# Optimization experiments

Measured on AMD Instinct MI355X. Metric: run time of the kernel, lower is better.

## Reference

```python
import jax, jax.numpy as jnp
import numpy as np

B, IN_SIZE, P = 16384, 4096, 8
D = IN_SIZE // P  # 512


def setup_inputs() -> dict:
    key = jax.random.key(0)
    ks = jax.random.split(key, 10)
    bound = 1.0 / np.sqrt(D)  # fan_in = int_dim
    return {
        "x": jax.random.normal(ks[0], (B, IN_SIZE), dtype=jnp.float32),
        "weights1": jax.random.uniform(ks[1], (P, D, D), jnp.float32, -bound, bound),
        "bias1": jax.random.uniform(ks[2], (IN_SIZE,), jnp.float32, -bound, bound),
        "weights2": jax.random.uniform(ks[3], (P, D, D), jnp.float32, -bound, bound),
        "bias2": jax.random.uniform(ks[4], (IN_SIZE,), jnp.float32, -bound, bound),
        # trainable swish params (init 0 as in torch code)
        "gamma1": jnp.zeros((IN_SIZE,), jnp.float32),
        "beta1": jnp.zeros((IN_SIZE,), jnp.float32),
        "gamma3": jnp.zeros((IN_SIZE,), jnp.float32),
        "beta3": jnp.zeros((IN_SIZE,), jnp.float32),
        # Affine norms (scalar gain/bias)
        "gain1": jnp.ones((1,), jnp.float32),
        "nbias1": jnp.zeros((1,), jnp.float32),
        "gain3": jnp.ones((1,), jnp.float32),
        "nbias3": jnp.zeros((1,), jnp.float32),
    }


def _swish(x, gamma, beta):
    # f(x) = (gamma + sigmoid(beta*x) * (1-gamma)) * x
    return (gamma + jax.nn.sigmoid(beta * x) * (1.0 - gamma)) * x


def _block_matmul(x, w):
    # x: [B, IN_SIZE] -> [B, P, D]; block-diagonal matmul == batched per-partition GEMM
    xb = x.reshape(x.shape[0], P, D)
    return jnp.einsum("bpd,pde->bpe", xb, w).reshape(x.shape[0], IN_SIZE)


def reference(x, weights1, bias1, weights2, bias2, gamma1, beta1, gamma3, beta3,
              gain1, nbias1, gain3, nbias3):
    o1 = _swish(_block_matmul(x * gain1 + nbias1, weights1) + bias1, gamma1, beta1)
    o2 = _swish(_block_matmul(o1 * gain3 + nbias3, weights2) + bias2, gamma3, beta3) + x
    return o2
```

## Files before the change

### kernel.cpp

```cpp
#include <hip/hip_runtime.h>
#include <cstdint>
#include <cstddef>


#define B_ROWS 16384
#define IN_SZ  4096
#define P_PART 8
#define D_DIM  512

typedef unsigned short ushort_t;
typedef __attribute__((ext_vector_type(8))) short short8;
typedef __attribute__((ext_vector_type(4))) float f32x4;

__device__ inline unsigned short f2bf(float f) {
  union { float f; unsigned int u; } c; c.f = f;
  unsigned int u = c.u;
  return (unsigned short)((u + 0x7fffu + ((u >> 16) & 1u)) >> 16);
}

__device__ inline void gld_to_lds16(const void* g, void* l) {
  __builtin_amdgcn_global_load_lds((const __attribute__((address_space(1))) void*)g,
                                   (__attribute__((address_space(3))) void*)l,
                                   16, 0, 0);
}

__global__ __launch_bounds__(256) void wconv_kernel(const float* __restrict__ w1,
                                                    const float* __restrict__ w2,
                                                    ushort_t* __restrict__ wt1,
                                                    ushort_t* __restrict__ wt2) {
  __shared__ float tile[64][68];
  const int p = blockIdx.z & 7;
  const float*  src = (blockIdx.z < 8) ? w1 : w2;
  ushort_t*     dst = (blockIdx.z < 8) ? wt1 : wt2;
  const int k0 = blockIdx.x * 64;
  const int n0 = blockIdx.y * 64;
  const int t = threadIdx.x;

  const float* base = src + ((size_t)p * D_DIM + k0) * D_DIM + n0;
#pragma unroll
  for (int i = 0; i < 4; ++i) {
    int f = t + i * 256;
    int kr = f >> 4;
    int c4 = f & 15;
    float4 v = *(const float4*)(base + (size_t)kr * D_DIM + c4 * 4);
    *(float4*)(&tile[kr][c4 * 4]) = v;
  }
  __syncthreads();
  ushort_t* obase = dst + ((size_t)p * D_DIM + n0) * D_DIM + k0;
#pragma unroll
  for (int i = 0; i < 4; ++i) {
    int f = t + i * 256;
    int nr = f >> 4;
    int kc = (f & 15) * 4;
    unsigned int lo = f2bf(tile[kc + 0][nr]) | ((unsigned int)f2bf(tile[kc + 1][nr]) << 16);
    unsigned int hi = f2bf(tile[kc + 2][nr]) | ((unsigned int)f2bf(tile[kc + 3][nr]) << 16);
    uint2 pk; pk.x = lo; pk.y = hi;
    *(uint2*)(obase + (size_t)nr * D_DIM + kc) = pk;
  }
}

__global__ __launch_bounds__(256) void gemm1_kernel(
    const float* __restrict__ x, const ushort_t* __restrict__ wt1,
    const float* __restrict__ bias1, const float* __restrict__ gamma1,
    const float* __restrict__ beta1,
    const float* __restrict__ gain1, const float* __restrict__ nbias1,
    const float* __restrict__ gain3, const float* __restrict__ nbias3,
    ushort_t* __restrict__ o1) {
  __shared__ __align__(16) ushort_t As[128 * 64];
  __shared__ __align__(16) ushort_t Bs[128 * 64];

  const int t = threadIdx.x;
  const int lane = t & 63, wid = t >> 6;
  const int wm = wid & 1, wn = wid >> 1;
  const int l15 = lane & 15, quad = lane >> 4;
  const int m0 = blockIdx.x * 128;
  const int n0 = blockIdx.y * 128;
  const int p  = blockIdx.z;

  const float g1 = gain1[0], nb1 = nbias1[0];
  const float g3 = gain3[0], nb3 = nbias3[0];

  f32x4 acc[4][4];
#pragma unroll
  for (int i = 0; i < 4; ++i)
#pragma unroll
    for (int j = 0; j < 4; ++j) acc[i][j] = (f32x4)(0.0f);

  const ushort_t* wbase = wt1 + (size_t)p * D_DIM * D_DIM;

  for (int kt = 0; kt < 8; ++kt) {
    __syncthreads();
    const float* xtile = x + (size_t)m0 * IN_SZ + p * D_DIM + kt * 64;
#pragma unroll
    for (int i = 0; i < 8; ++i) {
      int f = t + i * 256;
      int row = f >> 4, c4 = f & 15;
      float4 v = *(const float4*)(xtile + (size_t)row * IN_SZ + c4 * 4);
      v.x = v.x * g1 + nb1; v.y = v.y * g1 + nb1;
      v.z = v.z * g1 + nb1; v.w = v.w * g1 + nb1;
      uint2 pk;
      pk.x = f2bf(v.x) | ((unsigned int)f2bf(v.y) << 16);
      pk.y = f2bf(v.z) | ((unsigned int)f2bf(v.w) << 16);
      *(uint2*)(&As[f * 4]) = pk;
    }
#pragma unroll
    for (int c = 0; c < 4; ++c) {
      int off = (wid * 4 + c) * 1024;
      int lb = off + lane * 16;
      int n = lb >> 7, kb = lb & 127;
      const ushort_t* g = wbase + (size_t)(n0 + n) * D_DIM + kt * 64 + (kb >> 1);
      gld_to_lds16(g, (char*)Bs + off);
    }
    __syncthreads();
#pragma unroll
    for (int kk = 0; kk < 2; ++kk) {
      const int kof = kk * 32 + quad * 8;
      short8 a[4], b[4];
#pragma unroll
      for (int i = 0; i < 4; ++i)
        a[i] = *(const short8*)(&As[(wm * 64 + i * 16 + l15) * 64 + kof]);
#pragma unroll
      for (int j = 0; j < 4; ++j)
        b[j] = *(const short8*)(&Bs[(wn * 64 + j * 16 + l15) * 64 + kof]);
#pragma unroll
      for (int i = 0; i < 4; ++i)
#pragma unroll
        for (int j = 0; j < 4; ++j)
          acc[i][j] = __builtin_amdgcn_mfma_f32_16x16x32_bf16(a[i], b[j], acc[i][j], 0, 0, 0);
    }
  }

  const int colg0 = p * D_DIM + n0 + wn * 64;
  const int row0 = m0 + wm * 64 + quad * 4;
#pragma unroll
  for (int j = 0; j < 4; ++j) {
    int col = colg0 + j * 16 + l15;
    float bv = bias1[col], ga = gamma1[col], be = beta1[col];
#pragma unroll
    for (int i = 0; i < 4; ++i) {
      int r0 = row0 + i * 16;
#pragma unroll
      for (int r = 0; r < 4; ++r) {
        float v = acc[i][j][r] + bv;
        float sg = 1.0f / (1.0f + __expf(-be * v));
        float o = (ga + sg * (1.0f - ga)) * v;
        o = o * g3 + nb3;
        o1[(size_t)(r0 + r) * IN_SZ + col] = f2bf(o);
      }
    }
  }
}

__global__ __launch_bounds__(256) void gemm2_kernel(
    const ushort_t* __restrict__ o1, const ushort_t* __restrict__ wt2,
    const float* __restrict__ bias2, const float* __restrict__ gamma3,
    const float* __restrict__ beta3,
    const float* __restrict__ x, float* __restrict__ out) {
  __shared__ __align__(16) ushort_t As[128 * 64];
  __shared__ __align__(16) ushort_t Bs[128 * 64];

  const int t = threadIdx.x;
  const int lane = t & 63, wid = t >> 6;
  const int wm = wid & 1, wn = wid >> 1;
  const int l15 = lane & 15, quad = lane >> 4;
  const int m0 = blockIdx.x * 128;
  const int n0 = blockIdx.y * 128;
  const int p  = blockIdx.z;

  f32x4 acc[4][4];
#pragma unroll
  for (int i = 0; i < 4; ++i)
#pragma unroll
    for (int j = 0; j < 4; ++j) acc[i][j] = (f32x4)(0.0f);

  const ushort_t* wbase = wt2 + (size_t)p * D_DIM * D_DIM;

  for (int kt = 0; kt < 8; ++kt) {
    __syncthreads();
#pragma unroll
    for (int c = 0; c < 4; ++c) {
      int off = (wid * 4 + c) * 1024;
      int lb = off + lane * 16;
      int m = lb >> 7, kb = lb & 127;
      const ushort_t* g = o1 + (size_t)(m0 + m) * IN_SZ + p * D_DIM + kt * 64 + (kb >> 1);
      gld_to_lds16(g, (char*)As + off);
    }
#pragma unroll
    for (int c = 0; c < 4; ++c) {
      int off = (wid * 4 + c) * 1024;
      int lb = off + lane * 16;
      int n = lb >> 7, kb = lb & 127;
      const ushort_t* g = wbase + (size_t)(n0 + n) * D_DIM + kt * 64 + (kb >> 1);
      gld_to_lds16(g, (char*)Bs + off);
    }
    __syncthreads();
#pragma unroll
    for (int kk = 0; kk < 2; ++kk) {
      const int kof = kk * 32 + quad * 8;
      short8 a[4], b[4];
#pragma unroll
      for (int i = 0; i < 4; ++i)
        a[i] = *(const short8*)(&As[(wm * 64 + i * 16 + l15) * 64 + kof]);
#pragma unroll
      for (int j = 0; j < 4; ++j)
        b[j] = *(const short8*)(&Bs[(wn * 64 + j * 16 + l15) * 64 + kof]);
#pragma unroll
      for (int i = 0; i < 4; ++i)
#pragma unroll
        for (int j = 0; j < 4; ++j)
          acc[i][j] = __builtin_amdgcn_mfma_f32_16x16x32_bf16(a[i], b[j], acc[i][j], 0, 0, 0);
    }
  }

  const int colg0 = p * D_DIM + n0 + wn * 64;
  const int row0 = m0 + wm * 64 + quad * 4;
#pragma unroll
  for (int j = 0; j < 4; ++j) {
    int col = colg0 + j * 16 + l15;
    float bv = bias2[col], ga = gamma3[col], be = beta3[col];
#pragma unroll
    for (int i = 0; i < 4; ++i) {
      int r0 = row0 + i * 16;
#pragma unroll
      for (int r = 0; r < 4; ++r) {
        float v = acc[i][j][r] + bv;
        float sg = 1.0f / (1.0f + __expf(-be * v));
        float o = (ga + sg * (1.0f - ga)) * v;
        size_t idx = (size_t)(r0 + r) * IN_SZ + col;
        out[idx] = o + x[idx];
      }
    }
  }
}

extern "C" void kernel_launch(void* const* d_in, const int* in_sizes, int n_in,
                              void* d_out, int out_size, void* d_ws, size_t ws_size,
                              hipStream_t stream) {
  const float* x      = (const float*)d_in[0];
  const float* w1     = (const float*)d_in[1];
  const float* b1     = (const float*)d_in[2];
  const float* w2     = (const float*)d_in[3];
  const float* b2     = (const float*)d_in[4];
  const float* gamma1 = (const float*)d_in[5];
  const float* beta1  = (const float*)d_in[6];
  const float* gamma3 = (const float*)d_in[7];
  const float* beta3  = (const float*)d_in[8];
  const float* gain1  = (const float*)d_in[9];
  const float* nbias1 = (const float*)d_in[10];
  const float* gain3  = (const float*)d_in[11];
  const float* nbias3 = (const float*)d_in[12];
  float* out = (float*)d_out;

  ushort_t* o1  = (ushort_t*)d_ws;
  ushort_t* wt1 = (ushort_t*)((char*)d_ws + (size_t)B_ROWS * IN_SZ * 2);
  ushort_t* wt2 = wt1 + (size_t)P_PART * D_DIM * D_DIM;

  wconv_kernel<<<dim3(8, 8, 16), 256, 0, stream>>>(w1, w2, wt1, wt2);
  gemm1_kernel<<<dim3(128, 4, 8), 256, 0, stream>>>(x, wt1, b1, gamma1, beta1,
                                                    gain1, nbias1, gain3, nbias3, o1);
  gemm2_kernel<<<dim3(128, 4, 8), 256, 0, stream>>>(o1, wt2, b2, gamma3, beta3, x, out);
}
```

Before: 846.4 us.

## Fuse both block GEMMs into one kernel keeping intermediate activations in LDS

Replaces the two separate GEMM kernels with a single fused kernel. Each 512-thread block owns a 64-row slab of one partition and keeps the full 64x512 bf16 activation tile in swizzled shared memory. The first GEMM's swish output is written back into that same LDS buffer and used as the A operand of the second GEMM. This removes the bf16 intermediate round trip through global memory and one kernel launch. In exchange, weights are read directly from global/L2 into registers with no LDS staging, and each block's 64KB LDS footprint limits occupancy.

```diff
diff --git a/kernel.cpp b/kernel.cpp
--- a/kernel.cpp
+++ b/kernel.cpp
@@ -7,6 +7,7 @@
 #define IN_SZ  4096
 #define P_PART 8
 #define D_DIM  512
+#define M_BLK  64
 
 typedef unsigned short ushort_t;
 typedef __attribute__((ext_vector_type(8))) short short8;
@@ -18,11 +19,7 @@
   return (unsigned short)((u + 0x7fffu + ((u >> 16) & 1u)) >> 16);
 }
 
-__device__ inline void gld_to_lds16(const void* g, void* l) {
-  __builtin_amdgcn_global_load_lds((const __attribute__((address_space(1))) void*)g,
-                                   (__attribute__((address_space(3))) void*)l,
-                                   16, 0, 0);
-}
+__device__ inline int swz(int m, int c) { return m * D_DIM + (c ^ ((m & 7) << 3)); }
 
 __global__ __launch_bounds__(256) void wconv_kernel(const float* __restrict__ w1,
                                                     const float* __restrict__ w2,
@@ -59,174 +56,145 @@
   }
 }
 
-__global__ __launch_bounds__(256) void gemm1_kernel(
-    const float* __restrict__ x, const ushort_t* __restrict__ wt1,
+__global__ __launch_bounds__(512, 4) void fused_kernel(
+    const float* __restrict__ x,
+    const ushort_t* __restrict__ wt1, const ushort_t* __restrict__ wt2,
     const float* __restrict__ bias1, const float* __restrict__ gamma1,
     const float* __restrict__ beta1,
+    const float* __restrict__ bias2, const float* __restrict__ gamma3,
+    const float* __restrict__ beta3,
     const float* __restrict__ gain1, const float* __restrict__ nbias1,
     const float* __restrict__ gain3, const float* __restrict__ nbias3,
-    ushort_t* __restrict__ o1) {
-  __shared__ __align__(16) ushort_t As[128 * 64];
-  __shared__ __align__(16) ushort_t Bs[128 * 64];
+    float* __restrict__ out) {
+  __shared__ __align__(16) ushort_t Xs[M_BLK * D_DIM];
 
   const int t = threadIdx.x;
-  const int lane = t & 63, wid = t >> 6;
-  const int wm = wid & 1, wn = wid >> 1;
+  const int lane = t & 63, wn = t >> 6;
   const int l15 = lane & 15, quad = lane >> 4;
-  const int m0 = blockIdx.x * 128;
-  const int n0 = blockIdx.y * 128;
-  const int p  = blockIdx.z;
+  const int p  = blockIdx.x;
+  const int m0 = blockIdx.y * M_BLK;
 
   const float g1 = gain1[0], nb1 = nbias1[0];
   const float g3 = gain3[0], nb3 = nbias3[0];
 
+  {
+    const float* xb = x + (size_t)m0 * IN_SZ + (size_t)p * D_DIM;
+#pragma unroll
+    for (int i = 0; i < 16; ++i) {
+      int g = t + i * 512;
+      int m = g >> 7;
+      int c = (g & 127) * 4;
+      float4 v = *(const float4*)(xb + (size_t)m * IN_SZ + c);
+      uint2 pk;
+      pk.x = f2bf(v.x * g1 + nb1) | ((unsigned int)f2bf(v.y * g1 + nb1) << 16);
+      pk.y = f2bf(v.z * g1 + nb1) | ((unsigned int)f2bf(v.w * g1 + nb1) << 16);
+      *(uint2*)(&Xs[swz(m, c)]) = pk;
+    }
+  }
+  __syncthreads();
+
   f32x4 acc[4][4];
 #pragma unroll
   for (int i = 0; i < 4; ++i)
 #pragma unroll
     for (int j = 0; j < 4; ++j) acc[i][j] = (f32x4)(0.0f);
 
-  const ushort_t* wbase = wt1 + (size_t)p * D_DIM * D_DIM;
-
-  for (int kt = 0; kt < 8; ++kt) {
-    __syncthreads();
-    const float* xtile = x + (size_t)m0 * IN_SZ + p * D_DIM + kt * 64;
-#pragma unroll
-    for (int i = 0; i < 8; ++i) {
-      int f = t + i * 256;
-      int row = f >> 4, c4 = f & 15;
-      float4 v = *(const float4*)(xtile + (size_t)row * IN_SZ + c4 * 4);
-      v.x = v.x * g1 + nb1; v.y = v.y * g1 + nb1;
-      v.z = v.z * g1 + nb1; v.w = v.w * g1 + nb1;
+  {
+    const ushort_t* w1b = wt1 + (size_t)p * D_DIM * D_DIM
+                              + (size_t)(wn * 64 + l15) * D_DIM;
+#pragma unroll 2
+    for (int kt = 0; kt < 8; ++kt) {
+#pragma unroll
+      for (int kk = 0; kk < 2; ++kk) {
+        const int kof = kt * 64 + kk * 32 + quad * 8;
+        short8 a[4], b[4];
+#pragma unroll
+        for (int i = 0; i < 4; ++i)
+          a[i] = *(const short8*)(w1b + (size_t)(i * 16) * D_DIM + kof);
+#pragma unroll
+        for (int j = 0; j < 4; ++j)
+          b[j] = *(const short8*)(&Xs[swz(j * 16 + l15, kof)]);
+#pragma unroll
+        for (int i = 0; i < 4; ++i)
+#pragma unroll
+          for (int j = 0; j < 4; ++j)
+            acc[i][j] = __builtin_amdgcn_mfma_f32_16x16x32_bf16(a[i], b[j], acc[i][j], 0, 0, 0);
+      }
+    }
+  }
+
+  __syncthreads();
+
+#pragma unroll
+  for (int i = 0; i < 4; ++i) {
+    const int n = wn * 64 + i * 16 + quad * 4;
+    const int col = p * D_DIM + n;
+    const float4 bv = *(const float4*)(bias1 + col);
+    const float4 ga = *(const float4*)(gamma1 + col);
+    const float4 be = *(const float4*)(beta1 + col);
+#pragma unroll
+    for (int j = 0; j < 4; ++j) {
+      const int m = j * 16 + l15;
+      float o[4];
+#pragma unroll
+      for (int r = 0; r < 4; ++r) {
+        float v = acc[i][j][r] + ((const float*)&bv)[r];
+        float g = ((const float*)&ga)[r];
+        float sg = 1.0f / (1.0f + __expf(-((const float*)&be)[r] * v));
+        o[r] = ((g + sg * (1.0f - g)) * v) * g3 + nb3;
+      }
       uint2 pk;
-      pk.x = f2bf(v.x) | ((unsigned int)f2bf(v.y) << 16);
-      pk.y = f2bf(v.z) | ((unsigned int)f2bf(v.w) << 16);
-      *(uint2*)(&As[f * 4]) = pk;
-    }
-#pragma unroll
-    for (int c = 0; c < 4; ++c) {
-      int off = (wid * 4 + c) * 1024;
-      int lb = off + lane * 16;
-      int n = lb >> 7, kb = lb & 127;
-      const ushort_t* g = wbase + (size_t)(n0 + n) * D_DIM + kt * 64 + (kb >> 1);
-      gld_to_lds16(g, (char*)Bs + off);
-    }
-    __syncthreads();
-#pragma unroll
-    for (int kk = 0; kk < 2; ++kk) {
-      const int kof = kk * 32 + quad * 8;
-      short8 a[4], b[4];
-#pragma unroll
-      for (int i = 0; i < 4; ++i)
-        a[i] = *(const short8*)(&As[(wm * 64 + i * 16 + l15) * 64 + kof]);
-#pragma unroll
-      for (int j = 0; j < 4; ++j)
-        b[j] = *(const short8*)(&Bs[(wn * 64 + j * 16 + l15) * 64 + kof]);
-#pragma unroll
-      for (int i = 0; i < 4; ++i)
+      pk.x = f2bf(o[0]) | ((unsigned int)f2bf(o[1]) << 16);
+      pk.y = f2bf(o[2]) | ((unsigned int)f2bf(o[3]) << 16);
+      *(uint2*)(&Xs[swz(m, n)]) = pk;
+    }
+  }
+  __syncthreads();
+
+  f32x4 acc2[4][4];
+#pragma unroll
+  for (int i = 0; i < 4; ++i)
+#pragma unroll
+    for (int j = 0; j < 4; ++j) acc2[i][j] = (f32x4)(0.0f);
+
+  {
+    const ushort_t* w2b = wt2 + (size_t)p * D_DIM * D_DIM
+                              + (size_t)(wn * 64 + l15) * D_DIM;
+#pragma unroll 2
+    for (int kt = 0; kt < 8; ++kt) {
+#pragma unroll
+      for (int kk = 0; kk < 2; ++kk) {
+        const int kof = kt * 64 + kk * 32 + quad * 8;
+        short8 a[4], b[4];
+#pragma unroll
+        for (int i = 0; i < 4; ++i)
+          a[i] = *(const short8*)(&Xs[swz(i * 16 + l15, kof)]);
 #pragma unroll
         for (int j = 0; j < 4; ++j)
-          acc[i][j] = __builtin_amdgcn_mfma_f32_16x16x32_bf16(a[i], b[j], acc[i][j], 0, 0, 0);
-    }
-  }
-
-  const int colg0 = p * D_DIM + n0 + wn * 64;
-  const int row0 = m0 + wm * 64 + quad * 4;
+          b[j] = *(const short8*)(w2b + (size_t)(j * 16) * D_DIM + kof);
+#pragma unroll
+        for (int i = 0; i < 4; ++i)
+#pragma unroll
+          for (int j = 0; j < 4; ++j)
+            acc2[i][j] = __builtin_amdgcn_mfma_f32_16x16x32_bf16(a[i], b[j], acc2[i][j], 0, 0, 0);
+      }
+    }
+  }
+
+  const int colg0 = p * D_DIM + wn * 64;
 #pragma unroll
   for (int j = 0; j < 4; ++j) {
-    int col = colg0 + j * 16 + l15;
-    float bv = bias1[col], ga = gamma1[col], be = beta1[col];
+    const int col = colg0 + j * 16 + l15;
+    const float bv = bias2[col], ga = gamma3[col], be = beta3[col];
 #pragma unroll
     for (int i = 0; i < 4; ++i) {
-      int r0 = row0 + i * 16;
+      const int r0 = m0 + i * 16 + quad * 4;
 #pragma unroll
       for (int r = 0; r < 4; ++r) {
-        float v = acc[i][j][r] + bv;
+        float v = acc2[i][j][r] + bv;
         float sg = 1.0f / (1.0f + __expf(-be * v));
         float o = (ga + sg * (1.0f - ga)) * v;
-        o = o * g3 + nb3;
-        o1[(size_t)(r0 + r) * IN_SZ + col] = f2bf(o);
-      }
-    }
-  }
-}
-
-__global__ __launch_bounds__(256) void gemm2_kernel(
-    const ushort_t* __restrict__ o1, const ushort_t* __restrict__ wt2,
-    const float* __restrict__ bias2, const float* __restrict__ gamma3,
-    const float* __restrict__ beta3,
-    const float* __restrict__ x, float* __restrict__ out) {
-  __shared__ __align__(16) ushort_t As[128 * 64];
-  __shared__ __align__(16) ushort_t Bs[128 * 64];
-
-  const int t = threadIdx.x;
-  const int lane = t & 63, wid = t >> 6;
-  const int wm = wid & 1, wn = wid >> 1;
-  const int l15 = lane & 15, quad = lane >> 4;
-  const int m0 = blockIdx.x * 128;
-  const int n0 = blockIdx.y * 128;
-  const int p  = blockIdx.z;
-
-  f32x4 acc[4][4];
-#pragma unroll
-  for (int i = 0; i < 4; ++i)
-#pragma unroll
-    for (int j = 0; j < 4; ++j) acc[i][j] = (f32x4)(0.0f);
-
-  const ushort_t* wbase = wt2 + (size_t)p * D_DIM * D_DIM;
-
-  for (int kt = 0; kt < 8; ++kt) {
-    __syncthreads();
-#pragma unroll
-    for (int c = 0; c < 4; ++c) {
-      int off = (wid * 4 + c) * 1024;
-      int lb = off + lane * 16;
-      int m = lb >> 7, kb = lb & 127;
-      const ushort_t* g = o1 + (size_t)(m0 + m) * IN_SZ + p * D_DIM + kt * 64 + (kb >> 1);
-      gld_to_lds16(g, (char*)As + off);
-    }
-#pragma unroll
-    for (int c = 0; c < 4; ++c) {
-      int off = (wid * 4 + c) * 1024;
-      int lb = off + lane * 16;
-      int n = lb >> 7, kb = lb & 127;
-      const ushort_t* g = wbase + (size_t)(n0 + n) * D_DIM + kt * 64 + (kb >> 1);
-      gld_to_lds16(g, (char*)Bs + off);
-    }
-    __syncthreads();
-#pragma unroll
-    for (int kk = 0; kk < 2; ++kk) {
-      const int kof = kk * 32 + quad * 8;
-      short8 a[4], b[4];
-#pragma unroll
-      for (int i = 0; i < 4; ++i)
-        a[i] = *(const short8*)(&As[(wm * 64 + i * 16 + l15) * 64 + kof]);
-#pragma unroll
-      for (int j = 0; j < 4; ++j)
-        b[j] = *(const short8*)(&Bs[(wn * 64 + j * 16 + l15) * 64 + kof]);
-#pragma unroll
-      for (int i = 0; i < 4; ++i)
-#pragma unroll
-        for (int j = 0; j < 4; ++j)
-          acc[i][j] = __builtin_amdgcn_mfma_f32_16x16x32_bf16(a[i], b[j], acc[i][j], 0, 0, 0);
-    }
-  }
-
-  const int colg0 = p * D_DIM + n0 + wn * 64;
-  const int row0 = m0 + wm * 64 + quad * 4;
-#pragma unroll
-  for (int j = 0; j < 4; ++j) {
-    int col = colg0 + j * 16 + l15;
-    float bv = bias2[col], ga = gamma3[col], be = beta3[col];
-#pragma unroll
-    for (int i = 0; i < 4; ++i) {
-      int r0 = row0 + i * 16;
-#pragma unroll
-      for (int r = 0; r < 4; ++r) {
-        float v = acc[i][j][r] + bv;
-        float sg = 1.0f / (1.0f + __expf(-be * v));
-        float o = (ga + sg * (1.0f - ga)) * v;
-        size_t idx = (size_t)(r0 + r) * IN_SZ + col;
+        const size_t idx = (size_t)(r0 + r) * IN_SZ + col;
         out[idx] = o + x[idx];
       }
     }
@@ -251,12 +219,11 @@
   const float* nbias3 = (const float*)d_in[12];
   float* out = (float*)d_out;
 
-  ushort_t* o1  = (ushort_t*)d_ws;
-  ushort_t* wt1 = (ushort_t*)((char*)d_ws + (size_t)B_ROWS * IN_SZ * 2);
+  ushort_t* wt1 = (ushort_t*)d_ws;
   ushort_t* wt2 = wt1 + (size_t)P_PART * D_DIM * D_DIM;
 
   wconv_kernel<<<dim3(8, 8, 16), 256, 0, stream>>>(w1, w2, wt1, wt2);
-  gemm1_kernel<<<dim3(128, 4, 8), 256, 0, stream>>>(x, wt1, b1, gamma1, beta1,
-                                                    gain1, nbias1, gain3, nbias3, o1);
-  gemm2_kernel<<<dim3(128, 4, 8), 256, 0, stream>>>(o1, wt2, b2, gamma3, beta3, x, out);
-}
+  fused_kernel<<<dim3(P_PART, B_ROWS / M_BLK), 512, 0, stream>>>(
+      x, wt1, wt2, b1, gamma1, beta1, b2, gamma3, beta3,
+      gain1, nbias1, gain3, nbias3, out);
+}
```

Result: faster. 749.9 us (-11.4%).
